# Kernel tuning notes

Hardware: AMD Instinct MI355X
Metric: run time of the kernel (lower is better)

Reference implementation:

```python
import math
import jax, jax.numpy as jnp
import numpy as np

N_EMBD = 1024
N_HEAD = 16
NUM_BUCKETS = 32
MAX_DISTANCE = 128


def _relative_position_bucket(relative_position, num_buckets=NUM_BUCKETS, max_distance=MAX_DISTANCE):
    # unidirectional (bidirectional=False): rp = -min(rp, 0)
    rp = -jnp.minimum(relative_position, 0)
    max_exact = num_buckets // 2
    is_small = rp < max_exact
    rp_large = max_exact + (
        jnp.log(rp.astype(jnp.float32) / max_exact + 1e-10)
        / math.log(max_distance / max_exact)
        * (num_buckets - max_exact)
    ).astype(jnp.int32)
    rp_large = jnp.minimum(rp_large, num_buckets - 1)
    return jnp.where(is_small, rp, rp_large)


def setup_inputs() -> dict:
    key = jax.random.key(0)
    ks = jax.random.split(key, 6)
    B, T, C = 4, 2048, N_EMBD
    s_in = 1.0 / math.sqrt(C)
    x = jax.random.normal(ks[0], (B, T, C), dtype=jnp.float32)
    W_attn = jax.random.normal(ks[1], (3 * C, C), dtype=jnp.float32) * s_in
    b_attn = jnp.zeros((3 * C,), dtype=jnp.float32)
    W_proj = jax.random.normal(ks[2], (C, C), dtype=jnp.float32) * s_in
    b_proj = jnp.zeros((C,), dtype=jnp.float32)
    rel_emb = jax.random.normal(ks[3], (NUM_BUCKETS, N_HEAD), dtype=jnp.float32) * 0.02
    return {"x": x, "W_attn": W_attn, "b_attn": b_attn,
            "W_proj": W_proj, "b_proj": b_proj, "rel_emb": rel_emb}


def reference(x, W_attn, b_attn, W_proj, b_proj, rel_emb):
    B, T, C = x.shape
    H = N_HEAD
    D = C // H
    qkv = x @ W_attn.T + b_attn              # [B,T,3C]
    q, k, v = jnp.split(qkv, 3, axis=-1)
    q = q.reshape(B, T, H, D).transpose(0, 2, 1, 3)  # [B,H,T,D]
    k = k.reshape(B, T, H, D).transpose(0, 2, 1, 3)
    v = v.reshape(B, T, H, D).transpose(0, 2, 1, 3)

    # T5 relative position bias (unidirectional)
    pos = jnp.arange(T)
    rel_pos = pos[None, :] - pos[:, None]            # [T,T] key - query
    buckets = _relative_position_bucket(rel_pos)     # [T,T]
    rel_bias = rel_emb[buckets]                      # [T,T,H]
    rel_bias = rel_bias.transpose(2, 0, 1)[None]     # [1,H,T,T]

    att = jnp.einsum('bhqd,bhkd->bhqk', q, k) * (1.0 / math.sqrt(D))
    att = att + rel_bias
    causal = jnp.tril(jnp.ones((T, T), dtype=bool))
    att = jnp.where(causal[None, None], att, -jnp.inf)
    att = jax.nn.softmax(att, axis=-1)
    y = jnp.einsum('bhqk,bhkd->bhqd', att, v)        # [B,H,T,D]
    y = y.transpose(0, 2, 1, 3).reshape(B, T, C)
    y = y @ W_proj.T + b_proj
    return y
```

## Files before the change

### kernel.cpp

```cpp
#include <hip/hip_runtime.h>
#include <hip/hip_bf16.h>

typedef __attribute__((ext_vector_type(8))) short short8;
typedef __attribute__((ext_vector_type(4))) short short4v;
typedef __attribute__((ext_vector_type(4))) float f32x4;

#define DEVI static __device__ __forceinline__

#define MTOK 8192
#define CDIM 1024
#define HN 16
#define HD 64
#define TSEQ 2048

#if defined(__has_builtin)
#if __has_builtin(__builtin_amdgcn_exp2f)
#define EXP2(x) __builtin_amdgcn_exp2f(x)
#else
#define EXP2(x) exp2f(x)
#endif
#else
#define EXP2(x) exp2f(x)
#endif

DEVI short bf16_rne(float f) {
  union { float f; unsigned u; } v; v.f = f;
  unsigned r = v.u + 0x7FFFu + ((v.u >> 16) & 1u);
  return (short)(r >> 16);
}

DEVI unsigned cvt_pk_bf16(float lo, float hi) {
  unsigned r;
  asm("v_cvt_pk_bf16_f32 %0, %1, %2" : "=v"(r) : "v"(lo), "v"(hi));
  return r;
}

DEVI void gload16(const void* g, void* l) {
  __builtin_amdgcn_global_load_lds(
      (const __attribute__((address_space(1))) void*)(unsigned long long)g,
      (__attribute__((address_space(3))) void*)(unsigned long long)l, 16, 0, 0);
}

#define MFMA_B16(A,B,C) __builtin_amdgcn_mfma_f32_16x16x32_bf16(A,B,C,0,0,0)

__global__ void pack_kernel(const float* __restrict__ x, const float* __restrict__ Wa,
                            const float* __restrict__ Wp,
                            short* __restrict__ xb, short* __restrict__ wab,
                            short* __restrict__ wpb) {
  const int NX4 = MTOK*CDIM/4, NA4 = 3*CDIM*CDIM/4, NP4 = CDIM*CDIM/4;
  const int total = NX4 + NA4 + NP4;
  for (int i = blockIdx.x*blockDim.x + threadIdx.x; i < total; i += gridDim.x*blockDim.x) {
    const float* src; short* dst; int off;
    if (i < NX4)          { src = x;  dst = xb;  off = i*4; }
    else if (i < NX4+NA4) { src = Wa; dst = wab; off = (i-NX4)*4; }
    else                  { src = Wp; dst = wpb; off = (i-NX4-NA4)*4; }
    float4 v = *(const float4*)(src + off);
    short4v r;
    r.x = bf16_rne(v.x); r.y = bf16_rne(v.y); r.z = bf16_rne(v.z); r.w = bf16_rne(v.w);
    *(short4v*)(dst + off) = r;
  }
}

__global__ void bias_table_kernel(const float* __restrict__ rel_emb, float* __restrict__ tab) {
  int d = blockIdx.x*blockDim.x + threadIdx.x;
  if (d >= TSEQ) return;
  int bucket;
  if (d < 16) bucket = d;
  else {
    int bl = 16 + (int)(logf((float)d / 16.0f + 1e-10f) / 2.0794415416798357f * 16.0f);
    bucket = bl < 31 ? bl : 31;
  }
  for (int h = 0; h < HN; h++) tab[h*TSEQ + d] = rel_emb[bucket*HN + h];
}

template<int EPI>
__global__ __launch_bounds__(512)
void gemm2(const short* __restrict__ A, const short* __restrict__ B,
           const float* __restrict__ bias,
           short* __restrict__ oq, short* __restrict__ ok, short* __restrict__ vt,
           float* __restrict__ of) {
  const int K = CDIM;
  int nbx = gridDim.x;
  int idx = blockIdx.y * nbx + blockIdx.x;
  int cpx = (nbx * gridDim.y) >> 3;
  int sw = (idx & 7) * cpx + (idx >> 3);
  int n0 = (sw % nbx) * 128, m0 = (sw / nbx) * 256;

  int tid = threadIdx.x, lane = tid & 63, w = tid >> 6;
  int wm = w >> 1, wn = w & 1;
  int r16 = lane & 15, g = lane >> 4;

  __shared__ __align__(16) short As[3][256*32];
  __shared__ __align__(16) short Bs[3][128*32];

  f32x4 zf = {0.f,0.f,0.f,0.f};
  f32x4 acc[4][4];
  #pragma unroll
  for (int mf = 0; mf < 4; mf++)
    #pragma unroll
    for (int nf = 0; nf < 4; nf++) acc[mf][nf] = zf;

  int r0 = tid >> 2;
  int cswz = (((tid & 3) ^ ((r0 >> 1) & 3)) << 3);
  long long aofs = (long long)(m0 + r0) * K + cswz;
  long long bofs = (long long)(n0 + r0) * K + cswz;

  auto STAGE = [&](int kt, int bi) {
    gload16(A + aofs + kt*32,          (short*)As[bi] + tid*8);
    gload16(A + aofs + kt*32 + 128*K,  (short*)As[bi] + 4096 + tid*8);
    gload16(B + bofs + kt*32,          (short*)Bs[bi] + tid*8);
  };

  STAGE(0, 0); STAGE(1, 1);
  asm volatile("s_waitcnt vmcnt(3)" ::: "memory");
  __builtin_amdgcn_s_barrier();
  __builtin_amdgcn_sched_barrier(0);

  int swz3 = (r16 >> 1) & 3;
  int fbA = (wm*64 + r16)*32 + ((g ^ swz3) << 3);
  int fbB = (wn*64 + r16)*32 + ((g ^ swz3) << 3);

  for (int kt = 0; kt < 32; kt++) {
    int cur = kt % 3;
    if (kt < 30) STAGE(kt + 2, (kt + 2) % 3);
    const short* Ab = As[cur];
    const short* Bb = Bs[cur];
    short8 af[4], bf[4];
    #pragma unroll
    for (int mf = 0; mf < 4; mf++) af[mf] = *(const short8*)(Ab + fbA + mf*512);
    #pragma unroll
    for (int nf = 0; nf < 4; nf++) bf[nf] = *(const short8*)(Bb + fbB + nf*512);
    __builtin_amdgcn_s_setprio(1);
    #pragma unroll
    for (int mf = 0; mf < 4; mf++)
      #pragma unroll
      for (int nf = 0; nf < 4; nf++)
        acc[mf][nf] = MFMA_B16(af[mf], bf[nf], acc[mf][nf]);
    __builtin_amdgcn_s_setprio(0);
    if (kt < 30) asm volatile("s_waitcnt vmcnt(3)" ::: "memory");
    else         asm volatile("s_waitcnt vmcnt(0)" ::: "memory");
    __builtin_amdgcn_s_barrier();
    __builtin_amdgcn_sched_barrier(0);
  }

  int b = m0 >> 11;
  int mrel = (m0 & 2047) + wm*64 + g*4;
  if constexpr (EPI == 0) {
    int which = n0 >> 10;
    int hh = ((n0 & 1023) >> 6) + wn;
    long long bh = (long long)(b*HN + hh);
    #pragma unroll
    for (int nf = 0; nf < 4; nf++) {
      int dd = nf*16 + r16;
      float bv = bias[n0 + wn*64 + dd];
      if (which == 2) {
        short* vdst = vt + (bh*HD + dd)*TSEQ + mrel;
        #pragma unroll
        for (int mf = 0; mf < 4; mf++) {
          short4v pv;
          #pragma unroll
          for (int j = 0; j < 4; j++) pv[j] = bf16_rne(acc[mf][nf][j] + bv);
          *(short4v*)(vdst + mf*16) = pv;
        }
      } else {
        short* odst = (which == 0 ? oq : ok) + bh*TSEQ*HD + dd;
        #pragma unroll
        for (int mf = 0; mf < 4; mf++)
          #pragma unroll
          for (int j = 0; j < 4; j++)
            odst[(long long)(mrel + mf*16 + j)*HD] = bf16_rne(acc[mf][nf][j] + bv);
      }
    }
  } else {
    #pragma unroll
    for (int nf = 0; nf < 4; nf++) {
      int col = n0 + wn*64 + nf*16 + r16;
      float bv = bias[col];
      #pragma unroll
      for (int mf = 0; mf < 4; mf++)
        #pragma unroll
        for (int j = 0; j < 4; j++)
          of[(long long)(m0 + wm*64 + mf*16 + g*4 + j)*CDIM + col] = acc[mf][nf][j] + bv;
    }
  }
}

__global__ __launch_bounds__(256)
void attn_kernel(const short* __restrict__ Qg, const short* __restrict__ Kg,
                 const short* __restrict__ Vtg, const float* __restrict__ btab,
                 short* __restrict__ outp) {
  int bh = blockIdx.x;
  int qb = 15 - (int)blockIdx.y;
  int h = bh & (HN-1), b = bh >> 4;
  int q0 = qb * 128;
  int tid = threadIdx.x, lane = tid & 63, w = tid >> 6;
  int r16 = lane & 15, g = lane >> 4;

  __shared__ __align__(16) short Ks[2][64*64];
  __shared__ __align__(16) short Vs[2][64*64];
  __shared__ __align__(16) short Ps[8][1024];
  __shared__ float bias_s[256];

  bias_s[tid & 255] = btab[h*TSEQ + (tid & 255)] * 1.44269504f;
  float cb = btab[h*TSEQ + 255] * 1.44269504f;

  auto STAGE = [&](int t, int bi) {
    int kb = t * 64;
    #pragma unroll
    for (int i = 0; i < 2; i++) {
      int idx = tid + i*256;
      int r = idx >> 3;
      int cq = ((idx & 7) ^ (r & 7)) * 8;
      gload16(Kg  + ((long long)bh*TSEQ + kb + r)*HD + cq, (short*)Ks[bi] + idx*8);
      gload16(Vtg + ((long long)bh*HD  + r)*TSEQ + kb + cq, (short*)Vs[bi] + idx*8);
    }
  };

  short8 qa[2][2];
  #pragma unroll
  for (int mi = 0; mi < 2; mi++)
    #pragma unroll
    for (int ks = 0; ks < 2; ks++)
      qa[mi][ks] = *(const short8*)(Qg + ((long long)bh*TSEQ + q0 + w*32 + mi*16 + r16)*HD + ks*32 + g*8);

  f32x4 zf = {0.f,0.f,0.f,0.f};
  f32x4 o[2][4];
  #pragma unroll
  for (int mi = 0; mi < 2; mi++)
    #pragma unroll
    for (int c = 0; c < 4; c++) o[mi][c] = zf;
  float m_[2] = {-1e30f, -1e30f}, l_[2] = {0.f, 0.f};

  const short8 ones = {0x3f80,0x3f80,0x3f80,0x3f80,0x3f80,0x3f80,0x3f80,0x3f80};
  int qmax_wave = q0 + w*32 + 31;
  int swz = r16 & 7;
  int qrel = q0 + w*32 + r16;
  const float SC = 0.18033688f;
  int ntiles = (q0 + 128) >> 6;

  STAGE(0, 0);
  STAGE(1, 1);
  asm volatile("s_waitcnt lgkmcnt(0)" ::: "memory");

  for (int t = 0; t < ntiles; t++) {
    if (t + 1 < ntiles) asm volatile("s_waitcnt vmcnt(4)" ::: "memory");
    else                asm volatile("s_waitcnt vmcnt(0)" ::: "memory");
    __builtin_amdgcn_s_barrier();
    __builtin_amdgcn_sched_barrier(0);
    int kb = t * 64;
    const short* Kb = Ks[t & 1];
    const short* Vb = Vs[t & 1];
    if (kb <= qmax_wave) {
      f32x4 s[2][4];
      #pragma unroll
      for (int mi = 0; mi < 2; mi++)
        #pragma unroll
        for (int n = 0; n < 4; n++) s[mi][n] = zf;
      #pragma unroll
      for (int n = 0; n < 4; n++) {
        #pragma unroll
        for (int ks = 0; ks < 2; ks++) {
          short8 kf = *(const short8*)&Kb[(n*16 + r16)*64 + ((ks*4 + g) ^ swz)*8];
          s[0][n] = MFMA_B16(kf, qa[0][ks], s[0][n]);
          s[1][n] = MFMA_B16(kf, qa[1][ks], s[1][n]);
        }
      }
      bool far = (kb + 176 <= q0 + w*32);
      #pragma unroll
      for (int mi = 0; mi < 2; mi++) {
        char* prow = (char*)Ps[w*2 + mi] + r16*128 + ((g & 1) << 3);
        if (far) {
          float smax = s[mi][0][0];
          #pragma unroll
          for (int n = 0; n < 4; n++)
            #pragma unroll
            for (int j = 0; j < 4; j++) smax = fmaxf(smax, s[mi][n][j]);
          float mx = smax*SC + cb;
          mx = fmaxf(mx, __shfl_xor(mx, 16));
          mx = fmaxf(mx, __shfl_xor(mx, 32));
          float mnew;
          if (__all(mx <= m_[mi] + 8.0f)) {
            mnew = m_[mi];
          } else {
            mnew = fmaxf(m_[mi], mx);
            float corr = EXP2(m_[mi] - mnew);
            l_[mi] *= corr;
            #pragma unroll
            for (int c = 0; c < 4; c++) o[mi][c] *= corr;
            m_[mi] = mnew;
          }
          float cc = cb - mnew;
          #pragma unroll
          for (int n = 0; n < 4; n++) {
            unsigned u0 = cvt_pk_bf16(EXP2(__builtin_fmaf(s[mi][n][0], SC, cc)),
                                      EXP2(__builtin_fmaf(s[mi][n][1], SC, cc)));
            unsigned u1 = cvt_pk_bf16(EXP2(__builtin_fmaf(s[mi][n][2], SC, cc)),
                                      EXP2(__builtin_fmaf(s[mi][n][3], SC, cc)));
            *(uint2*)(prow + ((((n*2 + (g >> 1)) ^ swz)) << 4)) = make_uint2(u0, u1);
          }
        } else {
          int dbase = qrel + mi*16 - kb - g*4;
          float rowv[4][4];
          #pragma unroll
          for (int n = 0; n < 4; n++)
            #pragma unroll
            for (int j = 0; j < 4; j++) {
              int d = dbase - n*16 - j;
              rowv[n][j] = (d >= 0) ? s[mi][n][j]*SC + bias_s[d] : -1e30f;
            }
          float mx = rowv[0][0];
          #pragma unroll
          for (int n = 0; n < 4; n++)
            #pragma unroll
            for (int j = 0; j < 4; j++) mx = fmaxf(mx, rowv[n][j]);
          mx = fmaxf(mx, __shfl_xor(mx, 16));
          mx = fmaxf(mx, __shfl_xor(mx, 32));
          float mnew;
          if (__all(mx <= m_[mi] + 8.0f)) {
            mnew = m_[mi];
          } else {
            mnew = fmaxf(m_[mi], mx);
            float corr = EXP2(m_[mi] - mnew);
            l_[mi] *= corr;
            #pragma unroll
            for (int c = 0; c < 4; c++) o[mi][c] *= corr;
            m_[mi] = mnew;
          }
          #pragma unroll
          for (int n = 0; n < 4; n++) {
            unsigned u0 = cvt_pk_bf16(EXP2(rowv[n][0] - mnew), EXP2(rowv[n][1] - mnew));
            unsigned u1 = cvt_pk_bf16(EXP2(rowv[n][2] - mnew), EXP2(rowv[n][3] - mnew));
            *(uint2*)(prow + ((((n*2 + (g >> 1)) ^ swz)) << 4)) = make_uint2(u0, u1);
          }
        }
      }
      f32x4 lacc[2] = {zf, zf};
      #pragma unroll
      for (int ks = 0; ks < 2; ks++) {
        short8 pf0 = *(const short8*)((char*)Ps[w*2+0] + r16*128 + (((ks*4 + g) ^ swz) << 4));
        short8 pf1 = *(const short8*)((char*)Ps[w*2+1] + r16*128 + (((ks*4 + g) ^ swz) << 4));
        lacc[0] = MFMA_B16(ones, pf0, lacc[0]);
        lacc[1] = MFMA_B16(ones, pf1, lacc[1]);
        #pragma unroll
        for (int c = 0; c < 4; c++) {
          short8 vf = *(const short8*)&Vb[(c*16 + r16)*64 + ((ks*4 + g) ^ swz)*8];
          o[0][c] = MFMA_B16(vf, pf0, o[0][c]);
          o[1][c] = MFMA_B16(vf, pf1, o[1][c]);
        }
      }
      l_[0] += lacc[0][0];
      l_[1] += lacc[1][0];
    }
    __builtin_amdgcn_s_barrier();
    __builtin_amdgcn_sched_barrier(0);
    if (t + 2 < ntiles) STAGE(t + 2, t & 1);
  }

  #pragma unroll
  for (int mi = 0; mi < 2; mi++) {
    float inv = 1.0f / l_[mi];
    long long base = ((long long)(b*TSEQ + qrel + mi*16))*CDIM + h*HD;
    #pragma unroll
    for (int c = 0; c < 4; c++) {
      #pragma unroll
      for (int jj = 0; jj < 2; jj++) {
        unsigned pv = cvt_pk_bf16(o[mi][c][jj*2]*inv, o[mi][c][jj*2+1]*inv);
        *(unsigned*)(outp + base + c*16 + g*4 + jj*2) = pv;
      }
    }
  }
}

extern "C" void kernel_launch(void* const* d_in, const int* in_sizes, int n_in,
                              void* d_out, int out_size, void* d_ws, size_t ws_size,
                              hipStream_t stream) {
  (void)in_sizes; (void)n_in; (void)out_size; (void)ws_size;
  const float* x      = (const float*)d_in[0];
  const float* W_attn = (const float*)d_in[1];
  const float* b_attn = (const float*)d_in[2];
  const float* W_proj = (const float*)d_in[3];
  const float* b_proj = (const float*)d_in[4];
  const float* rel    = (const float*)d_in[5];
  float* out = (float*)d_out;
  char* ws = (char*)d_ws;

  short* xb   = (short*)(ws);
  short* wab  = (short*)(ws + 16777216LL);
  short* wpb  = (short*)(ws + 23068672LL);
  short* qbuf = (short*)(ws + 25165824LL);
  short* kbuf = (short*)(ws + 41943040LL);
  short* vt   = (short*)(ws + 58720256LL);
  short* att  = (short*)(ws + 75497472LL);
  float* tab  = (float*)(ws + 92274688LL);

  pack_kernel<<<2048, 256, 0, stream>>>(x, W_attn, W_proj, xb, wab, wpb);
  bias_table_kernel<<<8, 256, 0, stream>>>(rel, tab);
  gemm2<0><<<dim3(24, 32), 512, 0, stream>>>(xb, wab, b_attn, qbuf, kbuf, vt, nullptr);
  attn_kernel<<<dim3(64, 16), 256, 0, stream>>>(qbuf, kbuf, vt, tab, att);
  gemm2<1><<<dim3(8, 32), 512, 0, stream>>>(att, wpb, b_proj, nullptr, nullptr, nullptr, out);
}
```

Measured before the change: 255.1 us.

## Load V fragments directly from global in attention; shrink proj GEMM M-tile

```diff
diff --git a/kernel.cpp b/kernel.cpp
--- a/kernel.cpp
+++ b/kernel.cpp
@@ -73,32 +73,35 @@
   for (int h = 0; h < HN; h++) tab[h*TSEQ + d] = rel_emb[bucket*HN + h];
 }
 
-template<int EPI>
+template<int EPI, int MW>
 __global__ __launch_bounds__(512)
 void gemm2(const short* __restrict__ A, const short* __restrict__ B,
            const float* __restrict__ bias,
            short* __restrict__ oq, short* __restrict__ ok, short* __restrict__ vt,
            float* __restrict__ of) {
   const int K = CDIM;
+  constexpr int TM  = MW * 64;
+  constexpr int WNM = 8 / MW;
+  constexpr int NF  = 8 / WNM;
   int nbx = gridDim.x;
   int idx = blockIdx.y * nbx + blockIdx.x;
   int cpx = (nbx * gridDim.y) >> 3;
   int sw = (idx & 7) * cpx + (idx >> 3);
-  int n0 = (sw % nbx) * 128, m0 = (sw / nbx) * 256;
+  int n0 = (sw % nbx) * 128, m0 = (sw / nbx) * TM;
 
   int tid = threadIdx.x, lane = tid & 63, w = tid >> 6;
-  int wm = w >> 1, wn = w & 1;
+  int wm = w / WNM, wn = w % WNM;
   int r16 = lane & 15, g = lane >> 4;
 
-  __shared__ __align__(16) short As[3][256*32];
+  __shared__ __align__(16) short As[3][TM*32];
   __shared__ __align__(16) short Bs[3][128*32];
 
   f32x4 zf = {0.f,0.f,0.f,0.f};
-  f32x4 acc[4][4];
+  f32x4 acc[4][NF];
   #pragma unroll
   for (int mf = 0; mf < 4; mf++)
     #pragma unroll
-    for (int nf = 0; nf < 4; nf++) acc[mf][nf] = zf;
+    for (int nf = 0; nf < NF; nf++) acc[mf][nf] = zf;
 
   int r0 = tid >> 2;
   int cswz = (((tid & 3) ^ ((r0 >> 1) & 3)) << 3);
@@ -106,39 +109,45 @@
   long long bofs = (long long)(n0 + r0) * K + cswz;
 
   auto STAGE = [&](int kt, int bi) {
-    gload16(A + aofs + kt*32,          (short*)As[bi] + tid*8);
-    gload16(A + aofs + kt*32 + 128*K,  (short*)As[bi] + 4096 + tid*8);
-    gload16(B + bofs + kt*32,          (short*)Bs[bi] + tid*8);
+    #pragma unroll
+    for (int p = 0; p < MW/2; p++)
+      gload16(A + aofs + kt*32 + (long long)p*128*K, (short*)As[bi] + p*4096 + tid*8);
+    gload16(B + bofs + kt*32, (short*)Bs[bi] + tid*8);
   };
 
   STAGE(0, 0); STAGE(1, 1);
-  asm volatile("s_waitcnt vmcnt(3)" ::: "memory");
+  if constexpr (MW == 4) asm volatile("s_waitcnt vmcnt(3)" ::: "memory");
+  else                   asm volatile("s_waitcnt vmcnt(2)" ::: "memory");
   __builtin_amdgcn_s_barrier();
   __builtin_amdgcn_sched_barrier(0);
 
   int swz3 = (r16 >> 1) & 3;
   int fbA = (wm*64 + r16)*32 + ((g ^ swz3) << 3);
-  int fbB = (wn*64 + r16)*32 + ((g ^ swz3) << 3);
+  int fbB = (wn*(16*NF) + r16)*32 + ((g ^ swz3) << 3);
 
   for (int kt = 0; kt < 32; kt++) {
     int cur = kt % 3;
     if (kt < 30) STAGE(kt + 2, (kt + 2) % 3);
     const short* Ab = As[cur];
     const short* Bb = Bs[cur];
-    short8 af[4], bf[4];
+    short8 af[4], bf[NF];
     #pragma unroll
     for (int mf = 0; mf < 4; mf++) af[mf] = *(const short8*)(Ab + fbA + mf*512);
     #pragma unroll
-    for (int nf = 0; nf < 4; nf++) bf[nf] = *(const short8*)(Bb + fbB + nf*512);
+    for (int nf = 0; nf < NF; nf++) bf[nf] = *(const short8*)(Bb + fbB + nf*512);
     __builtin_amdgcn_s_setprio(1);
     #pragma unroll
     for (int mf = 0; mf < 4; mf++)
       #pragma unroll
-      for (int nf = 0; nf < 4; nf++)
+      for (int nf = 0; nf < NF; nf++)
         acc[mf][nf] = MFMA_B16(af[mf], bf[nf], acc[mf][nf]);
     __builtin_amdgcn_s_setprio(0);
-    if (kt < 30) asm volatile("s_waitcnt vmcnt(3)" ::: "memory");
-    else         asm volatile("s_waitcnt vmcnt(0)" ::: "memory");
+    if (kt < 30) {
+      if constexpr (MW == 4) asm volatile("s_waitcnt vmcnt(3)" ::: "memory");
+      else                   asm volatile("s_waitcnt vmcnt(2)" ::: "memory");
+    } else {
+      asm volatile("s_waitcnt vmcnt(0)" ::: "memory");
+    }
     __builtin_amdgcn_s_barrier();
     __builtin_amdgcn_sched_barrier(0);
   }
@@ -150,9 +159,9 @@
     int hh = ((n0 & 1023) >> 6) + wn;
     long long bh = (long long)(b*HN + hh);
     #pragma unroll
-    for (int nf = 0; nf < 4; nf++) {
+    for (int nf = 0; nf < NF; nf++) {
       int dd = nf*16 + r16;
-      float bv = bias[n0 + wn*64 + dd];
+      float bv = bias[n0 + wn*(16*NF) + dd];
       if (which == 2) {
         short* vdst = vt + (bh*HD + dd)*TSEQ + mrel;
         #pragma unroll
@@ -173,8 +182,8 @@
     }
   } else {
     #pragma unroll
-    for (int nf = 0; nf < 4; nf++) {
-      int col = n0 + wn*64 + nf*16 + r16;
+    for (int nf = 0; nf < NF; nf++) {
+      int col = n0 + wn*(16*NF) + nf*16 + r16;
       float bv = bias[col];
       #pragma unroll
       for (int mf = 0; mf < 4; mf++)
@@ -197,7 +206,6 @@
   int r16 = lane & 15, g = lane >> 4;
 
   __shared__ __align__(16) short Ks[2][64*64];
-  __shared__ __align__(16) short Vs[2][64*64];
   __shared__ __align__(16) short Ps[8][1024];
   __shared__ float bias_s[256];
 
@@ -211,10 +219,11 @@
       int idx = tid + i*256;
       int r = idx >> 3;
       int cq = ((idx & 7) ^ (r & 7)) * 8;
-      gload16(Kg  + ((long long)bh*TSEQ + kb + r)*HD + cq, (short*)Ks[bi] + idx*8);
-      gload16(Vtg + ((long long)bh*HD  + r)*TSEQ + kb + cq, (short*)Vs[bi] + idx*8);
+      gload16(Kg + ((long long)bh*TSEQ + kb + r)*HD + cq, (short*)Ks[bi] + idx*8);
     }
   };
+
+  const short* vgb = Vtg + (long long)bh*HD*TSEQ;
 
   short8 qa[2][2];
   #pragma unroll
@@ -243,14 +252,20 @@
   asm volatile("s_waitcnt lgkmcnt(0)" ::: "memory");
 
   for (int t = 0; t < ntiles; t++) {
-    if (t + 1 < ntiles) asm volatile("s_waitcnt vmcnt(4)" ::: "memory");
+    if (t + 1 < ntiles) asm volatile("s_waitcnt vmcnt(2)" ::: "memory");
     else                asm volatile("s_waitcnt vmcnt(0)" ::: "memory");
     __builtin_amdgcn_s_barrier();
     __builtin_amdgcn_sched_barrier(0);
     int kb = t * 64;
     const short* Kb = Ks[t & 1];
-    const short* Vb = Vs[t & 1];
     if (kb <= qmax_wave) {
+      short8 vf0[4], vf1[4];
+      #pragma unroll
+      for (int c = 0; c < 4; c++) {
+        const short* vrow = vgb + (long long)(c*16 + r16)*TSEQ + kb + g*8;
+        vf0[c] = *(const short8*)(vrow);
+        vf1[c] = *(const short8*)(vrow + 32);
+      }
       f32x4 s[2][4];
       #pragma unroll
       for (int mi = 0; mi < 2; mi++)
@@ -343,9 +358,9 @@
         lacc[1] = MFMA_B16(ones, pf1, lacc[1]);
         #pragma unroll
         for (int c = 0; c < 4; c++) {
-          short8 vf = *(const short8*)&Vb[(c*16 + r16)*64 + ((ks*4 + g) ^ swz)*8];
-          o[0][c] = MFMA_B16(vf, pf0, o[0][c]);
-          o[1][c] = MFMA_B16(vf, pf1, o[1][c]);
+          short8 vv = ks ? vf1[c] : vf0[c];
+          o[0][c] = MFMA_B16(vv, pf0, o[0][c]);
+          o[1][c] = MFMA_B16(vv, pf1, o[1][c]);
         }
       }
       l_[0] += lacc[0][0];
@@ -395,7 +410,7 @@
 
   pack_kernel<<<2048, 256, 0, stream>>>(x, W_attn, W_proj, xb, wab, wpb);
   bias_table_kernel<<<8, 256, 0, stream>>>(rel, tab);
-  gemm2<0><<<dim3(24, 32), 512, 0, stream>>>(xb, wab, b_attn, qbuf, kbuf, vt, nullptr);
+  gemm2<0,4><<<dim3(24, 32), 512, 0, stream>>>(xb, wab, b_attn, qbuf, kbuf, vt, nullptr);
   attn_kernel<<<dim3(64, 16), 256, 0, stream>>>(qbuf, kbuf, vt, tab, att);
-  gemm2<1><<<dim3(8, 32), 512, 0, stream>>>(att, wpb, b_proj, nullptr, nullptr, nullptr, out);
-}
+  gemm2<1,2><<<dim3(8, 64), 512, 0, stream>>>(att, wpb, b_proj, nullptr, nullptr, nullptr, out);
+}
```

New measurement: 281.3 us. 10.3% more time.
